# Performance work log

Measured on AMD Instinct MI355X. Metric: run time of the kernel, lower is better.

## Reference

```python
import jax, jax.numpy as jnp
import numpy as np

K = 16          # neighbors per query (args.k)
EPS_NORM = 1e-5  # LayerNorm / BatchNorm eps (torch default)


def _knn_edges(xyz, B, n):
    # batch-aware kNN: equal-sized batches, edges never cross batch boundary
    x = xyz.reshape(B, n, 3)
    d2 = jnp.sum((x[:, :, None, :] - x[:, None, :, :]) ** 2, -1)   # [B,n,n]
    _, idx = jax.lax.top_k(-d2, K)                                 # [B,n,K] local neighbor ids
    col = (idx + (jnp.arange(B) * n)[:, None, None]).reshape(-1)   # source (neighbor) [E]
    row = jnp.repeat(jnp.arange(B * n), K)                         # target (query)    [E]
    return row, col


def _forward(support_xyz, batch_index, features, lang_features, mask_flattened,
             W1, b1, ln_g, ln_b, W2, b2,
             Wl1, bl1, bn_g, bn_b, Wl2, bl2,
             Wr1, br1, Wr2, br2, row, col):
    N = support_xyz.shape[0]
    B, L, Fl = lang_features.shape
    # feat_encoder: Linear -> LayerNorm -> ReLU -> Linear
    h = features @ W1 + b1
    mu = h.mean(-1, keepdims=True)
    var = ((h - mu) ** 2).mean(-1, keepdims=True)
    h = (h - mu) / jnp.sqrt(var + EPS_NORM) * ln_g + ln_b
    feats = jax.nn.relu(h) @ W2 + b2                               # [N,F]
    # lang_encoder: Linear -> BatchNorm1d (batch statistics) -> ReLU -> Linear
    hl = lang_features.reshape(B * L, Fl) @ Wl1 + bl1
    mul = hl.mean(0)
    varl = ((hl - mul) ** 2).mean(0)
    hl = (hl - mul) / jnp.sqrt(varl + EPS_NORM) * bn_g + bn_b
    lang = (jax.nn.relu(hl) @ Wl2 + bl2).reshape(B, L, -1)         # [B,L,F]
    lang_flat = lang[batch_index]                                  # [N,L,F]
    # per-point / per-token attention logits
    atten = jnp.einsum('nf,nlf->nl', feats, lang_flat)             # [N,L]
    # segment softmax over incoming kNN edges (CenterOp max / add)
    attenmax = jax.ops.segment_max(atten[col], row, num_segments=N, indices_are_sorted=True)
    a = jnp.exp(atten[col] - attenmax[row])                        # [E,L]
    attensum = jax.ops.segment_sum(a, row, num_segments=N, indices_are_sorted=True)
    # CenterConv message
    att = a / attensum[row] * mask_flattened[row]                  # [E,L]
    att = att / (att.sum(-1, keepdims=True) + 1e-7)
    ctx = jnp.einsum('el,elf->ef', att, lang_flat[col])            # [E,F] attended lang feat
    xi, xj = support_xyz[row], support_xyz[col]
    d = xi - xj
    nrm = jnp.sqrt(jnp.sum(d * d, -1, keepdims=True) + 1e-12)
    ew = jnp.concatenate([xi, xj, d, nrm], -1)                     # [E,10]
    ew = jax.nn.relu(ew @ Wr1 + br1) @ Wr2 + br2                   # [E,F] rel_encoder
    msg = feats[col] * ctx * ew                                    # [E,F]
    rel = jax.ops.segment_sum(msg, row, num_segments=N, indices_are_sorted=True)
    return feats + rel


def setup_inputs() -> dict:
    key = jax.random.key(0)
    ks = jax.random.split(key, 12)
    B, n, L = 4, 1024, 16
    N = B * n
    Fv, Fl, F = 256, 768, 128
    def w(k, shp, fan):
        return jax.random.normal(k, shp, jnp.float32) / np.sqrt(fan).astype(np.float32)
    mask = (jax.random.uniform(ks[3], (N, L)) < 0.8).astype(jnp.float32).at[:, 0].set(1.0)
    return {
        'support_xyz': jax.random.normal(ks[0], (N, 3), jnp.float32),
        'batch_index': jnp.repeat(jnp.arange(B), n),
        'features': jax.random.normal(ks[1], (N, Fv), jnp.float32),
        'lang_features': jax.random.normal(ks[2], (B, L, Fl), jnp.float32),
        'mask_flattened': mask,
        'W1': w(ks[4], (Fv, F), Fv), 'b1': jnp.zeros(F, jnp.float32),
        'ln_g': jnp.ones(F, jnp.float32), 'ln_b': jnp.zeros(F, jnp.float32),
        'W2': w(ks[5], (F, F), F), 'b2': jnp.zeros(F, jnp.float32),
        'Wl1': w(ks[6], (Fl, F), Fl), 'bl1': jnp.zeros(F, jnp.float32),
        'bn_g': jnp.ones(F, jnp.float32), 'bn_b': jnp.zeros(F, jnp.float32),
        'Wl2': w(ks[7], (F, F), F), 'bl2': jnp.zeros(F, jnp.float32),
        'Wr1': w(ks[8], (10, 64), 10), 'br1': jnp.zeros(64, jnp.float32),
        'Wr2': w(ks[9], (64, F), 64), 'br2': jnp.zeros(F, jnp.float32),
    }


def reference(support_xyz, batch_index, features, lang_features, mask_flattened,
              W1, b1, ln_g, ln_b, W2, b2,
              Wl1, bl1, bn_g, bn_b, Wl2, bl2,
              Wr1, br1, Wr2, br2):
    B = lang_features.shape[0]
    n = support_xyz.shape[0] // B
    row, col = _knn_edges(support_xyz, B, n)
    return _forward(support_xyz, batch_index, features, lang_features, mask_flattened,
                    W1, b1, ln_g, ln_b, W2, b2,
                    Wl1, bl1, bn_g, bn_b, Wl2, bl2,
                    Wr1, br1, Wr2, br2, row, col)
```

## Files before the change

### kernel.cpp

```cpp
#include <hip/hip_runtime.h>

typedef unsigned long long u64;

#define N_PTS   4096
#define B_SZ    4
#define N_PER_B 1024
#define L_TOK   16
#define FV      256
#define FL      768
#define FDIM    128
#define KNN     16
#define RH      64

__global__ __launch_bounds__(256) void k1_kernel(const float* __restrict__ xyz,
                                                 const float* __restrict__ features,
                                                 const float* __restrict__ lf,
                                                 const float* __restrict__ W1,
                                                 const float* __restrict__ b1,
                                                 const float* __restrict__ ln_g,
                                                 const float* __restrict__ ln_b,
                                                 const float* __restrict__ W2,
                                                 const float* __restrict__ b2,
                                                 const float* __restrict__ Wl1,
                                                 const float* __restrict__ bl1,
                                                 int* __restrict__ knn,
                                                 float* __restrict__ feats,
                                                 float* __restrict__ hl) {
    __shared__ float smem[4 * 256 + 4 * 128 + 16];
    int b = blockIdx.x, t = threadIdx.x;

    if (b < 1024) {
        int lane = t & 63;
        int q = b * 4 + (t >> 6);
        int base = (q >> 10) << 10;
        float qx = xyz[q * 3 + 0];
        float qy = xyz[q * 3 + 1];
        float qz = xyz[q * 3 + 2];
        u64 keys[16];
#pragma unroll
        for (int m = 0; m < 16; m++) {
            int j = base + lane + (m << 6);
            float dx = qx - xyz[j * 3 + 0];
            float dy = qy - xyz[j * 3 + 1];
            float dz = qz - xyz[j * 3 + 2];
            float d2 = __fadd_rn(__fadd_rn(__fmul_rn(dx, dx), __fmul_rn(dy, dy)),
                                 __fmul_rn(dz, dz));
            keys[m] = (((u64)__float_as_uint(d2)) << 32) | (unsigned int)j;
        }
        for (int r = 0; r < KNN; r++) {
            u64 lmin = keys[0];
#pragma unroll
            for (int m = 1; m < 16; m++) lmin = (keys[m] < lmin) ? keys[m] : lmin;
            u64 g = lmin;
#pragma unroll
            for (int off = 32; off > 0; off >>= 1) {
                u64 o = __shfl_xor(g, off, 64);
                g = (o < g) ? o : g;
            }
#pragma unroll
            for (int m = 0; m < 16; m++)
                if (keys[m] == g) keys[m] = ~0ULL;
            if (lane == 0) knn[q * KNN + r] = (int)(g & 0xffffffffu);
        }
    } else if (b < 2048) {
        int i0 = (b - 1024) * 4;
        float* fin  = smem;
        float* rbuf = smem + 1024;
        float* red  = smem + 1536;
        for (int p = t; p < 4 * FV; p += 256) {
            int pp = p >> 8, k = p & 255;
            fin[pp * FV + k] = features[(i0 + pp) * FV + k];
        }
        __syncthreads();
        int c = t & 127, h = t >> 7;
        int p0 = 2 * h, p1 = 2 * h + 1;
        float bv = b1[c];
        float acc0 = bv, acc1 = bv;
        for (int k = 0; k < FV; k++) {
            float w = W1[k * FDIM + c];
            acc0 += fin[p0 * FV + k] * w;
            acc1 += fin[p1 * FV + k] * w;
        }
        float s0 = acc0, q0 = acc0 * acc0, s1 = acc1, q1 = acc1 * acc1;
#pragma unroll
        for (int off = 32; off > 0; off >>= 1) {
            s0 += __shfl_xor(s0, off, 64);
            q0 += __shfl_xor(q0, off, 64);
            s1 += __shfl_xor(s1, off, 64);
            q1 += __shfl_xor(q1, off, 64);
        }
        int wid = t >> 6;
        if ((t & 63) == 0) {
            red[wid * 4 + 0] = s0; red[wid * 4 + 1] = q0;
            red[wid * 4 + 2] = s1; red[wid * 4 + 3] = q1;
        }
        __syncthreads();
        float S0 = red[(2 * h) * 4 + 0] + red[(2 * h + 1) * 4 + 0];
        float Q0 = red[(2 * h) * 4 + 1] + red[(2 * h + 1) * 4 + 1];
        float S1 = red[(2 * h) * 4 + 2] + red[(2 * h + 1) * 4 + 2];
        float Q1 = red[(2 * h) * 4 + 3] + red[(2 * h + 1) * 4 + 3];
        float g = ln_g[c], bb = ln_b[c];
        float mu0 = S0 * (1.f / 128.f), var0 = Q0 * (1.f / 128.f) - mu0 * mu0;
        float mu1 = S1 * (1.f / 128.f), var1 = Q1 * (1.f / 128.f) - mu1 * mu1;
        float r0 = fmaxf((acc0 - mu0) * rsqrtf(var0 + 1e-5f) * g + bb, 0.f);
        float r1 = fmaxf((acc1 - mu1) * rsqrtf(var1 + 1e-5f) * g + bb, 0.f);
        rbuf[p0 * FDIM + c] = r0;
        rbuf[p1 * FDIM + c] = r1;
        __syncthreads();
        float b2v = b2[c];
        float f0 = b2v, f1 = b2v;
        for (int k = 0; k < FDIM; k++) {
            float w = W2[k * FDIM + c];
            f0 += rbuf[p0 * FDIM + k] * w;
            f1 += rbuf[p1 * FDIM + k] * w;
        }
        feats[(i0 + p0) * FDIM + c] = f0;
        feats[(i0 + p1) * FDIM + c] = f1;
    } else {
        int r = b - 2048;
        float* lrow = smem;
        float* part = smem + 768;
        for (int k = t; k < FL; k += 256) lrow[k] = lf[r * FL + k];
        __syncthreads();
        int c = t & 127, kh = t >> 7;
        float acc = (kh == 0) ? bl1[c] : 0.f;
        int k0 = kh * 384;
        for (int k = k0; k < k0 + 384; k++) acc += lrow[k] * Wl1[k * FDIM + c];
        part[kh * FDIM + c] = acc;
        __syncthreads();
        if (kh == 0) hl[r * FDIM + c] = part[c] + part[FDIM + c];
    }
}

__global__ __launch_bounds__(128) void lang2_kernel(const float* __restrict__ hl,
                                                    const float* __restrict__ bn_g,
                                                    const float* __restrict__ bn_b,
                                                    const float* __restrict__ Wl2,
                                                    const float* __restrict__ bl2,
                                                    float* __restrict__ lang) {
    __shared__ float rl4[4][FDIM];
    int t = threadIdx.x;
    int r0 = blockIdx.x * 4;
    float s = 0.f, s2 = 0.f;
    for (int r = 0; r < 64; r++) {
        float v = hl[r * FDIM + t];
        s += v; s2 += v * v;
    }
    float mu = s * (1.f / 64.f);
    float var = s2 * (1.f / 64.f) - mu * mu;
    float rs = rsqrtf(var + 1e-5f);
    float g = bn_g[t], bb = bn_b[t];
#pragma unroll
    for (int p = 0; p < 4; p++)
        rl4[p][t] = fmaxf((hl[(r0 + p) * FDIM + t] - mu) * rs * g + bb, 0.f);
    __syncthreads();
    float bv = bl2[t];
    float a0 = bv, a1 = bv, a2 = bv, a3 = bv;
    for (int k = 0; k < FDIM; k++) {
        float w = Wl2[k * FDIM + t];
        a0 += rl4[0][k] * w;
        a1 += rl4[1][k] * w;
        a2 += rl4[2][k] * w;
        a3 += rl4[3][k] * w;
    }
    lang[(r0 + 0) * FDIM + t] = a0;
    lang[(r0 + 1) * FDIM + t] = a1;
    lang[(r0 + 2) * FDIM + t] = a2;
    lang[(r0 + 3) * FDIM + t] = a3;
}

__global__ __launch_bounds__(256) void atten_kernel(const float* __restrict__ feats,
                                                    const float* __restrict__ lang,
                                                    float* __restrict__ atten) {
    __shared__ float fb[2][FDIM];
    __shared__ float pb[256];
    int t = threadIdx.x;
    int half = t >> 7, tt = t & 127;
    int i = blockIdx.x * 2 + half;
    fb[half][tt] = feats[i * FDIM + tt];
    __syncthreads();
    int l = tt >> 3, sj = tt & 7;
    int bi = i >> 10;
    const float* lrow = lang + (bi * L_TOK + l) * FDIM;
    float p = 0.f;
#pragma unroll
    for (int m = 0; m < 16; m++) {
        int k = sj + (m << 3);
        p += fb[half][k] * lrow[k];
    }
    pb[t] = p;
    __syncthreads();
    if (tt < L_TOK) {
        float a = 0.f;
#pragma unroll
        for (int u = 0; u < 8; u++) a += pb[half * 128 + tt * 8 + u];
        atten[i * L_TOK + tt] = a;
    }
}

__global__ __launch_bounds__(128) void edge_kernel(const float* __restrict__ xyz,
                                                   const float* __restrict__ mask,
                                                   const float* __restrict__ Wr1,
                                                   const float* __restrict__ br1,
                                                   const float* __restrict__ Wr2,
                                                   const float* __restrict__ br2,
                                                   const int* __restrict__ knn,
                                                   const float* __restrict__ lang,
                                                   const float* __restrict__ feats,
                                                   const float* __restrict__ atten,
                                                   float* __restrict__ out) {
    __shared__ int   idx[KNN];
    __shared__ float sat[KNN][L_TOK];
    __shared__ float satt[KNN][L_TOK];
    __shared__ float ein[KNN][12];
    __shared__ float hid[KNN][RH];
    int i = blockIdx.x, t = threadIdx.x;
    int bi = i >> 10;
    if (t < KNN) idx[t] = knn[i * KNN + t];
    float lsreg[L_TOK];
    const float* lb = lang + bi * L_TOK * FDIM + t;
#pragma unroll
    for (int l = 0; l < L_TOK; l++) lsreg[l] = lb[l * FDIM];
    float wreg[RH];
#pragma unroll
    for (int k = 0; k < RH; k++) wreg[k] = Wr2[k * FDIM + t];
    __syncthreads();
    for (int p = t; p < KNN * L_TOK; p += 128) {
        int e = p >> 4, l = p & 15;
        sat[e][l] = atten[idx[e] * L_TOK + l];
    }
    __syncthreads();
    if (t < L_TOK) {
        int l = t;
        float m = -1e30f;
        for (int e = 0; e < KNN; e++) m = fmaxf(m, sat[e][l]);
        float sum = 0.f;
        for (int e = 0; e < KNN; e++) {
            float a = expf(sat[e][l] - m);
            satt[e][l] = a;
            sum += a;
        }
        float inv = mask[i * L_TOK + l] / sum;
        for (int e = 0; e < KNN; e++) satt[e][l] *= inv;
    }
    __syncthreads();
    if (t < KNN) {
        int e = t;
        float s = 0.f;
        for (int l = 0; l < L_TOK; l++) s += satt[e][l];
        float inv = 1.f / (s + 1e-7f);
        for (int l = 0; l < L_TOK; l++) satt[e][l] *= inv;
        int j = idx[e];
        float xi0 = xyz[i * 3 + 0], xi1 = xyz[i * 3 + 1], xi2 = xyz[i * 3 + 2];
        float xj0 = xyz[j * 3 + 0], xj1 = xyz[j * 3 + 1], xj2 = xyz[j * 3 + 2];
        float d0 = xi0 - xj0, d1 = xi1 - xj1, d2v = xi2 - xj2;
        float nr = sqrtf(d0 * d0 + d1 * d1 + d2v * d2v + 1e-12f);
        ein[e][0] = xi0; ein[e][1] = xi1; ein[e][2] = xi2;
        ein[e][3] = xj0; ein[e][4] = xj1; ein[e][5] = xj2;
        ein[e][6] = d0;  ein[e][7] = d1;  ein[e][8] = d2v;
        ein[e][9] = nr;
    }
    __syncthreads();
    for (int p = t; p < KNN * RH; p += 128) {
        int e = p >> 6, hd = p & 63;
        float a = br1[hd];
#pragma unroll
        for (int k = 0; k < 10; k++) a += ein[e][k] * Wr1[k * RH + hd];
        hid[e][hd] = fmaxf(a, 0.f);
    }
    __syncthreads();
    float fj[KNN];
#pragma unroll
    for (int e = 0; e < KNN; e++) fj[e] = feats[idx[e] * FDIM + t];
    float br2v = br2[t];
    float acc = 0.f;
#pragma unroll 4
    for (int e = 0; e < KNN; e++) {
        const float4* hp = (const float4*)(&hid[e][0]);
        const float4* sp = (const float4*)(&satt[e][0]);
        float ew = br2v;
#pragma unroll
        for (int k4 = 0; k4 < RH / 4; k4++) {
            float4 h4 = hp[k4];
            ew += h4.x * wreg[k4 * 4 + 0] + h4.y * wreg[k4 * 4 + 1]
                + h4.z * wreg[k4 * 4 + 2] + h4.w * wreg[k4 * 4 + 3];
        }
        float ctx = 0.f;
#pragma unroll
        for (int l4 = 0; l4 < 4; l4++) {
            float4 s4 = sp[l4];
            ctx += s4.x * lsreg[l4 * 4 + 0] + s4.y * lsreg[l4 * 4 + 1]
                 + s4.z * lsreg[l4 * 4 + 2] + s4.w * lsreg[l4 * 4 + 3];
        }
        acc += fj[e] * ctx * ew;
    }
    out[i * FDIM + t] = feats[i * FDIM + t] + acc;
}

extern "C" void kernel_launch(void* const* d_in, const int* in_sizes, int n_in,
                              void* d_out, int out_size, void* d_ws, size_t ws_size,
                              hipStream_t stream) {
    const float* xyz   = (const float*)d_in[0];
    const float* features = (const float*)d_in[2];
    const float* lang_f   = (const float*)d_in[3];
    const float* mask     = (const float*)d_in[4];
    const float* W1   = (const float*)d_in[5];
    const float* b1   = (const float*)d_in[6];
    const float* ln_g = (const float*)d_in[7];
    const float* ln_b = (const float*)d_in[8];
    const float* W2   = (const float*)d_in[9];
    const float* b2   = (const float*)d_in[10];
    const float* Wl1  = (const float*)d_in[11];
    const float* bl1  = (const float*)d_in[12];
    const float* bn_g = (const float*)d_in[13];
    const float* bn_b = (const float*)d_in[14];
    const float* Wl2  = (const float*)d_in[15];
    const float* bl2  = (const float*)d_in[16];
    const float* Wr1  = (const float*)d_in[17];
    const float* br1  = (const float*)d_in[18];
    const float* Wr2  = (const float*)d_in[19];
    const float* br2  = (const float*)d_in[20];

    float* ws_feats = (float*)d_ws;
    float* ws_atten = ws_feats + N_PTS * FDIM;
    float* ws_lang  = ws_atten + N_PTS * L_TOK;
    float* ws_hl    = ws_lang + B_SZ * L_TOK * FDIM;
    int*   ws_knn   = (int*)(ws_hl + 64 * FDIM);

    k1_kernel<<<2112, 256, 0, stream>>>(xyz, features, lang_f,
                                        W1, b1, ln_g, ln_b, W2, b2,
                                        Wl1, bl1, ws_knn, ws_feats, ws_hl);
    lang2_kernel<<<16, 128, 0, stream>>>(ws_hl, bn_g, bn_b, Wl2, bl2, ws_lang);
    atten_kernel<<<N_PTS / 2, 256, 0, stream>>>(ws_feats, ws_lang, ws_atten);
    edge_kernel<<<N_PTS, 128, 0, stream>>>(xyz, mask, Wr1, br1, Wr2, br2,
                                           ws_knn, ws_lang, ws_feats, ws_atten,
                                           (float*)d_out);
}
```

Before: 194.5 us.

## Rewrite edge kernel as one wavefront per point using bf16 MFMA

The edge kernel now gives each point a single 64-lane wavefront, with four points per block, and drops shared memory and block barriers. The segment softmax runs with register shuffles. The relative-position MLP second layer and the attention-weighted language context are computed with 16x16x32 bf16 MFMA instructions instead of scalar FMA loops. Wr2 and lang are converted to bf16 on the fly, which lowers precision and repeats the conversion in every wavefront. Half of the K dimension in the context MFMA is zero padding.

```diff
diff --git a/kernel.cpp b/kernel.cpp
--- a/kernel.cpp
+++ b/kernel.cpp
@@ -1,6 +1,8 @@
 #include <hip/hip_runtime.h>
 
 typedef unsigned long long u64;
+typedef short short8 __attribute__((ext_vector_type(8)));
+typedef float f32x4 __attribute__((ext_vector_type(4)));
 
 #define N_PTS   4096
 #define B_SZ    4
@@ -11,6 +13,12 @@
 #define FDIM    128
 #define KNN     16
 #define RH      64
+
+__device__ __forceinline__ short f2bf(float f) {
+    unsigned int x = __float_as_uint(f);
+    unsigned int r = (x + 0x7fffu + ((x >> 16) & 1u)) >> 16;
+    return (short)r;
+}
 
 __global__ __launch_bounds__(256) void k1_kernel(const float* __restrict__ xyz,
                                                  const float* __restrict__ features,
@@ -198,7 +206,7 @@
     }
 }
 
-__global__ __launch_bounds__(128) void edge_kernel(const float* __restrict__ xyz,
+__global__ __launch_bounds__(256) void edge_kernel(const float* __restrict__ xyz,
                                                    const float* __restrict__ mask,
                                                    const float* __restrict__ Wr1,
                                                    const float* __restrict__ br1,
@@ -209,92 +217,127 @@
                                                    const float* __restrict__ feats,
                                                    const float* __restrict__ atten,
                                                    float* __restrict__ out) {
-    __shared__ int   idx[KNN];
-    __shared__ float sat[KNN][L_TOK];
-    __shared__ float satt[KNN][L_TOK];
-    __shared__ float ein[KNN][12];
-    __shared__ float hid[KNN][RH];
-    int i = blockIdx.x, t = threadIdx.x;
-    int bi = i >> 10;
-    if (t < KNN) idx[t] = knn[i * KNN + t];
-    float lsreg[L_TOK];
-    const float* lb = lang + bi * L_TOK * FDIM + t;
-#pragma unroll
-    for (int l = 0; l < L_TOK; l++) lsreg[l] = lb[l * FDIM];
-    float wreg[RH];
-#pragma unroll
-    for (int k = 0; k < RH; k++) wreg[k] = Wr2[k * FDIM + t];
-    __syncthreads();
-    for (int p = t; p < KNN * L_TOK; p += 128) {
-        int e = p >> 4, l = p & 15;
-        sat[e][l] = atten[idx[e] * L_TOK + l];
-    }
-    __syncthreads();
-    if (t < L_TOK) {
-        int l = t;
-        float m = -1e30f;
-        for (int e = 0; e < KNN; e++) m = fmaxf(m, sat[e][l]);
-        float sum = 0.f;
-        for (int e = 0; e < KNN; e++) {
-            float a = expf(sat[e][l] - m);
-            satt[e][l] = a;
-            sum += a;
-        }
-        float inv = mask[i * L_TOK + l] / sum;
-        for (int e = 0; e < KNN; e++) satt[e][l] *= inv;
-    }
-    __syncthreads();
-    if (t < KNN) {
-        int e = t;
-        float s = 0.f;
-        for (int l = 0; l < L_TOK; l++) s += satt[e][l];
-        float inv = 1.f / (s + 1e-7f);
-        for (int l = 0; l < L_TOK; l++) satt[e][l] *= inv;
-        int j = idx[e];
-        float xi0 = xyz[i * 3 + 0], xi1 = xyz[i * 3 + 1], xi2 = xyz[i * 3 + 2];
-        float xj0 = xyz[j * 3 + 0], xj1 = xyz[j * 3 + 1], xj2 = xyz[j * 3 + 2];
-        float d0 = xi0 - xj0, d1 = xi1 - xj1, d2v = xi2 - xj2;
-        float nr = sqrtf(d0 * d0 + d1 * d1 + d2v * d2v + 1e-12f);
-        ein[e][0] = xi0; ein[e][1] = xi1; ein[e][2] = xi2;
-        ein[e][3] = xj0; ein[e][4] = xj1; ein[e][5] = xj2;
-        ein[e][6] = d0;  ein[e][7] = d1;  ein[e][8] = d2v;
-        ein[e][9] = nr;
-    }
-    __syncthreads();
-    for (int p = t; p < KNN * RH; p += 128) {
-        int e = p >> 6, hd = p & 63;
-        float a = br1[hd];
-#pragma unroll
-        for (int k = 0; k < 10; k++) a += ein[e][k] * Wr1[k * RH + hd];
-        hid[e][hd] = fmaxf(a, 0.f);
-    }
-    __syncthreads();
-    float fj[KNN];
-#pragma unroll
-    for (int e = 0; e < KNN; e++) fj[e] = feats[idx[e] * FDIM + t];
-    float br2v = br2[t];
-    float acc = 0.f;
-#pragma unroll 4
-    for (int e = 0; e < KNN; e++) {
-        const float4* hp = (const float4*)(&hid[e][0]);
-        const float4* sp = (const float4*)(&satt[e][0]);
-        float ew = br2v;
-#pragma unroll
-        for (int k4 = 0; k4 < RH / 4; k4++) {
-            float4 h4 = hp[k4];
-            ew += h4.x * wreg[k4 * 4 + 0] + h4.y * wreg[k4 * 4 + 1]
-                + h4.z * wreg[k4 * 4 + 2] + h4.w * wreg[k4 * 4 + 3];
-        }
-        float ctx = 0.f;
-#pragma unroll
-        for (int l4 = 0; l4 < 4; l4++) {
-            float4 s4 = sp[l4];
-            ctx += s4.x * lsreg[l4 * 4 + 0] + s4.y * lsreg[l4 * 4 + 1]
-                 + s4.z * lsreg[l4 * 4 + 2] + s4.w * lsreg[l4 * 4 + 3];
-        }
-        acc += fj[e] * ctx * ew;
-    }
-    out[i * FDIM + t] = feats[i * FDIM + t] + acc;
+    int lane = threadIdx.x & 63;
+    int wid  = threadIdx.x >> 6;
+    int i    = blockIdx.x * 4 + wid;
+    int bi   = i >> 10;
+    int quad = lane >> 4;
+    int e16  = lane & 15;
+
+    int idxe = knn[i * KNN + e16];
+
+    float sat[8];
+    if (quad < 2) {
+        const float4* ap = (const float4*)(atten + idxe * L_TOK + quad * 8);
+        float4 a0 = ap[0], a1 = ap[1];
+        sat[0] = a0.x; sat[1] = a0.y; sat[2] = a0.z; sat[3] = a0.w;
+        sat[4] = a1.x; sat[5] = a1.y; sat[6] = a1.z; sat[7] = a1.w;
+    } else {
+#pragma unroll
+        for (int j = 0; j < 8; j++) sat[j] = 0.f;
+    }
+
+    float mx[8];
+#pragma unroll
+    for (int j = 0; j < 8; j++) mx[j] = sat[j];
+#pragma unroll
+    for (int off = 1; off < 16; off <<= 1) {
+#pragma unroll
+        for (int j = 0; j < 8; j++) mx[j] = fmaxf(mx[j], __shfl_xor(mx[j], off, 16));
+    }
+    float ex[8], sm[8];
+#pragma unroll
+    for (int j = 0; j < 8; j++) { ex[j] = __expf(sat[j] - mx[j]); sm[j] = ex[j]; }
+#pragma unroll
+    for (int off = 1; off < 16; off <<= 1) {
+#pragma unroll
+        for (int j = 0; j < 8; j++) sm[j] += __shfl_xor(sm[j], off, 16);
+    }
+    float st[8];
+    if (quad < 2) {
+        const float4* mp = (const float4*)(mask + i * L_TOK + quad * 8);
+        float4 m0 = mp[0], m1 = mp[1];
+        float mv[8] = {m0.x, m0.y, m0.z, m0.w, m1.x, m1.y, m1.z, m1.w};
+#pragma unroll
+        for (int j = 0; j < 8; j++) st[j] = ex[j] * (mv[j] / sm[j]);
+    } else {
+#pragma unroll
+        for (int j = 0; j < 8; j++) st[j] = 0.f;
+    }
+    float s = st[0] + st[1] + st[2] + st[3] + st[4] + st[5] + st[6] + st[7];
+    s += __shfl_xor(s, 16, 64);
+    s += __shfl_xor(s, 32, 64);
+    float inv2 = 1.f / (s + 1e-7f);
+    short8 sattA;
+#pragma unroll
+    for (int j = 0; j < 8; j++) sattA[j] = f2bf(st[j] * inv2);
+
+    float xi0 = xyz[i * 3 + 0], xi1 = xyz[i * 3 + 1], xi2 = xyz[i * 3 + 2];
+    float xj0 = xyz[idxe * 3 + 0], xj1 = xyz[idxe * 3 + 1], xj2 = xyz[idxe * 3 + 2];
+    float d0 = xi0 - xj0, d1 = xi1 - xj1, d2v = xi2 - xj2;
+    float nr = sqrtf(d0 * d0 + d1 * d1 + d2v * d2v + 1e-12f);
+    float ein[10] = {xi0, xi1, xi2, xj0, xj1, xj2, d0, d1, d2v, nr};
+    short8 hidA[2];
+#pragma unroll
+    for (int sstep = 0; sstep < 2; sstep++) {
+        int k0 = sstep * 32 + quad * 8;
+        float h[8];
+        const float4* bp = (const float4*)(br1 + k0);
+        float4 b0 = bp[0], b1v = bp[1];
+        h[0] = b0.x; h[1] = b0.y; h[2] = b0.z; h[3] = b0.w;
+        h[4] = b1v.x; h[5] = b1v.y; h[6] = b1v.z; h[7] = b1v.w;
+#pragma unroll
+        for (int m = 0; m < 10; m++) {
+            const float4* wp = (const float4*)(Wr1 + m * RH + k0);
+            float4 w0 = wp[0], w1 = wp[1];
+            float em = ein[m];
+            h[0] += em * w0.x; h[1] += em * w0.y; h[2] += em * w0.z; h[3] += em * w0.w;
+            h[4] += em * w1.x; h[5] += em * w1.y; h[6] += em * w1.z; h[7] += em * w1.w;
+        }
+#pragma unroll
+        for (int j = 0; j < 8; j++) hidA[sstep][j] = f2bf(fmaxf(h[j], 0.f));
+    }
+
+    int idxr[4];
+#pragma unroll
+    for (int r = 0; r < 4; r++) idxr[r] = knn[i * KNN + quad * 4 + r];
+
+#pragma unroll 2
+    for (int tile = 0; tile < 8; tile++) {
+        int cc = tile * 16 + e16;
+        f32x4 accew = {0.f, 0.f, 0.f, 0.f};
+#pragma unroll
+        for (int sstep = 0; sstep < 2; sstep++) {
+            short8 w2B;
+#pragma unroll
+            for (int j = 0; j < 8; j++)
+                w2B[j] = f2bf(Wr2[(sstep * 32 + quad * 8 + j) * FDIM + cc]);
+            accew = __builtin_amdgcn_mfma_f32_16x16x32_bf16(hidA[sstep], w2B, accew, 0, 0, 0);
+        }
+        short8 lsB;
+        if (quad < 2) {
+#pragma unroll
+            for (int j = 0; j < 8; j++)
+                lsB[j] = f2bf(lang[bi * L_TOK * FDIM + (quad * 8 + j) * FDIM + cc]);
+        } else {
+#pragma unroll
+            for (int j = 0; j < 8; j++) lsB[j] = 0;
+        }
+        f32x4 accctx = {0.f, 0.f, 0.f, 0.f};
+        accctx = __builtin_amdgcn_mfma_f32_16x16x32_bf16(sattA, lsB, accctx, 0, 0, 0);
+
+        float br2c = br2[cc];
+        float msum = 0.f;
+#pragma unroll
+        for (int r = 0; r < 4; r++) {
+            float fj = feats[idxr[r] * FDIM + cc];
+            msum += fj * accctx[r] * (accew[r] + br2c);
+        }
+        msum += __shfl_xor(msum, 16, 64);
+        msum += __shfl_xor(msum, 32, 64);
+        if (lane < 16)
+            out[i * FDIM + cc] = feats[i * FDIM + cc] + msum;
+    }
 }
 
 extern "C" void kernel_launch(void* const* d_in, const int* in_sizes, int n_in,
@@ -332,7 +375,7 @@
                                         Wl1, bl1, ws_knn, ws_feats, ws_hl);
     lang2_kernel<<<16, 128, 0, stream>>>(ws_hl, bn_g, bn_b, Wl2, bl2, ws_lang);
     atten_kernel<<<N_PTS / 2, 256, 0, stream>>>(ws_feats, ws_lang, ws_atten);
-    edge_kernel<<<N_PTS, 128, 0, stream>>>(xyz, mask, Wr1, br1, Wr2, br2,
-                                           ws_knn, ws_lang, ws_feats, ws_atten,
-                                           (float*)d_out);
-}
+    edge_kernel<<<N_PTS / 4, 256, 0, stream>>>(xyz, mask, Wr1, br1, Wr2, br2,
+                                               ws_knn, ws_lang, ws_feats, ws_atten,
+                                               (float*)d_out);
+}
```

After: 165.7 us. 1.17x faster.
